# Kernel tuning notes

Hardware: AMD Instinct MI355X
Metric: run time of the kernel (lower is better)

## Reference

```python
import jax, jax.numpy as jnp
import numpy as np

HEADS = 16
D_MODEL = 2048
HEAD_DIM = D_MODEL // HEADS


def setup_inputs() -> dict:
    key = jax.random.key(0)
    ks = jax.random.split(key, 8)
    s = 1.0 / np.sqrt(D_MODEL)
    return {
        "hidden_states": jax.random.normal(ks[0], (2, 2048, D_MODEL), jnp.float32),
        "Wq": jax.random.normal(ks[1], (D_MODEL, D_MODEL), jnp.float32) * s,
        "bq": jax.random.normal(ks[2], (D_MODEL,), jnp.float32) * s,
        "Wk": jax.random.normal(ks[3], (D_MODEL, D_MODEL), jnp.float32) * s,
        "Wv": jax.random.normal(ks[4], (D_MODEL, D_MODEL), jnp.float32) * s,
        "bv": jax.random.normal(ks[5], (D_MODEL,), jnp.float32) * s,
        "Wo": jax.random.normal(ks[6], (D_MODEL, D_MODEL), jnp.float32) * s,
        "bo": jax.random.normal(ks[7], (D_MODEL,), jnp.float32) * s,
    }


def reference(hidden_states, Wq, bq, Wk, Wv, bv, Wo, bo):
    bsz, q_len, _ = hidden_states.shape
    # torch Linear: y = x @ W^T + b; k_W has no bias
    q = hidden_states @ Wq.T + bq
    k = hidden_states @ Wk.T
    v = hidden_states @ Wv.T + bv
    # [b, h, s, d]
    def split_heads(t):
        return t.reshape(bsz, q_len, HEADS, HEAD_DIM).transpose(0, 2, 1, 3)
    q, k, v = split_heads(q), split_heads(k), split_heads(v)
    scale = 1.0 / np.sqrt(HEAD_DIM).astype(np.float32)
    attn_weights = jnp.einsum("bhqd,bhkd->bhqk", q, k) * scale
    attn_weights = jax.nn.softmax(attn_weights, axis=-1)
    attn_output = jnp.einsum("bhqk,bhkd->bhqd", attn_weights, v)
    attn_output = attn_output.transpose(0, 2, 1, 3).reshape(bsz, q_len, D_MODEL)
    attn_output = attn_output @ Wo.T + bo
    return attn_output, attn_weights
```

## Files before the change

kernel.cpp:

```cpp
#include <hip/hip_runtime.h>

typedef _Float16 f16;
typedef _Float16 f16x4 __attribute__((ext_vector_type(4)));
typedef _Float16 f16x8 __attribute__((ext_vector_type(8)));
typedef float f32x4 __attribute__((ext_vector_type(4)));

#define DM 2048
#define NT 4096
#define SEQ 2048
#define HD 128
#define NBH 32
#define QSCALE (0.08838834764831845f * 1.4426950408889634f)

__device__ __forceinline__ void gload16(const f16* g, f16* l) {
  __builtin_amdgcn_global_load_lds(
      (const __attribute__((address_space(1))) void*)g,
      (__attribute__((address_space(3))) void*)l, 16, 0, 0);
}

#define LGKM0                                        \
  asm volatile("s_waitcnt lgkmcnt(0)" ::: "memory"); \
  __builtin_amdgcn_sched_barrier(0)
#define VMC6                                       \
  asm volatile("s_waitcnt vmcnt(6)" ::: "memory"); \
  __builtin_amdgcn_sched_barrier(0)
#define VMC4                                       \
  asm volatile("s_waitcnt vmcnt(4)" ::: "memory"); \
  __builtin_amdgcn_sched_barrier(0)
#define VMC0                                       \
  asm volatile("s_waitcnt vmcnt(0)" ::: "memory"); \
  __builtin_amdgcn_sched_barrier(0)

__global__ __launch_bounds__(256) void cvt_f32_f16(const float* __restrict__ src,
                                                   f16* __restrict__ dst, int n4) {
  int i = blockIdx.x * 256 + threadIdx.x;
  int st = gridDim.x * 256;
  for (; i < n4; i += st) {
    float4 v = ((const float4*)src)[i];
    f16x4 h = {(f16)v.x, (f16)v.y, (f16)v.z, (f16)v.w};
    ((f16x4*)dst)[i] = h;
  }
}

__global__ __launch_bounds__(256) void cvt4_f32_f16(const float* __restrict__ hs,
                                                    const float* __restrict__ s0,
                                                    const float* __restrict__ s1,
                                                    const float* __restrict__ s2,
                                                    f16* __restrict__ hsd,
                                                    f16* __restrict__ wd) {
  int i = blockIdx.x * 256 + threadIdx.x;
  int st = gridDim.x * 256;
  for (; i < 5 * 1048576; i += st) {
    float4 v;
    f16x4 h;
    if (i < 2 * 1048576) {
      v = ((const float4*)hs)[i];
      h[0] = (f16)v.x; h[1] = (f16)v.y; h[2] = (f16)v.z; h[3] = (f16)v.w;
      ((f16x4*)hsd)[i] = h;
    } else {
      const int j = i - 2 * 1048576;
      const int r = j >> 20, jj = j & 1048575;
      const float* s = (r == 0) ? s0 : ((r == 1) ? s1 : s2);
      v = ((const float4*)s)[jj];
      h[0] = (f16)v.x; h[1] = (f16)v.y; h[2] = (f16)v.z; h[3] = (f16)v.w;
      ((f16x4*)wd)[j] = h;
    }
  }
}

template <int MODE>
__global__ __launch_bounds__(512, 2) void gemm8(const f16* __restrict__ A,
                                                const f16* __restrict__ Bm,
                                                const float* __restrict__ bias1,
                                                const float* __restrict__ bias2,
                                                float* __restrict__ outF,
                                                f16* __restrict__ outQ,
                                                f16* __restrict__ outK,
                                                f16* __restrict__ outV) {
  __shared__ __align__(16) f16 smem[73728];
  const int tid = threadIdx.x;
  const int w = tid >> 6, l = tid & 63;
  const int wr = w >> 2, wc = w & 3;
  const int sl = l & 15, t4 = l >> 4;

  const int nbx = gridDim.x;
  const int flat = blockIdx.y * nbx + blockIdx.x;
  const int chunk = (nbx * gridDim.y) >> 3;
  const int swz = (flat & 7) * chunk + (flat >> 3);
  const int row0 = (swz / nbx) * 128, col0 = (swz % nbx) * 256;

  f32x4 acc[4][4] = {};

  const int sr8 = l >> 3;
  const int sch = (l & 7) ^ (sr8 & 7);
  const f16* gA0 = A + (size_t)(row0 + w * 8 + sr8) * DM + sch * 8;
  const f16* gB0 = Bm + (size_t)(col0 + w * 8 + sr8) * DM + sch * 8;

#define SA(tb, kt, r) \
  gload16(gA0 + (size_t)(r) * 64 * DM + (kt) * 64, smem + (tb) * 8192 + (r) * 4096 + w * 512)
#define SB(tb, kt, r)                               \
  gload16(gB0 + (size_t)(r) * 64 * DM + (kt) * 64, \
          smem + 24576 + (tb) * 16384 + (r) * 4096 + w * 512)
#define MF(mi, ni, av, bv) \
  acc[mi][ni] = __builtin_amdgcn_mfma_f32_16x16x32_f16(av, bv, acc[mi][ni], 0, 0, 0)

  const int sx = sl & 7;
  const int sk0 = (t4 ^ sx) * 8;
  const int sk1 = ((4 + t4) ^ sx) * 8;
  const int arow = (wr * 64 + sl) * 64;
  const int brow = (wc * 64 + sl) * 64;

  SA(0, 0, 0); SA(0, 0, 1);
  SB(0, 0, 0); SB(0, 0, 1); SB(0, 0, 2); SB(0, 0, 3);
  SA(1, 1, 0); SA(1, 1, 1);
  SB(1, 1, 0); SB(1, 1, 1); SB(1, 1, 2); SB(1, 1, 3);
  VMC6;
  __builtin_amdgcn_s_barrier();

  int cur = 0;
#pragma unroll 1
  for (int t = 0; t < 32; ++t) {
    const int nb = (cur == 0) ? 2 : cur - 1;
    const bool pf = (t + 2 < 32);
    const int ab = cur * 8192;
    const int bb = 24576 + cur * 16384;
    f16x8 b0, b1, b2, b3, a0, a1;

    b0 = *(const f16x8*)&smem[bb + brow + sk0];
    b1 = *(const f16x8*)&smem[bb + brow + 1024 + sk0];
    b2 = *(const f16x8*)&smem[bb + brow + 2048 + sk0];
    b3 = *(const f16x8*)&smem[bb + brow + 3072 + sk0];
    a0 = *(const f16x8*)&smem[ab + arow + sk0];
    a1 = *(const f16x8*)&smem[ab + arow + 1024 + sk0];
    if (pf) { SA(nb, t + 2, 0); SA(nb, t + 2, 1); }
    __builtin_amdgcn_s_barrier();
    LGKM0;
    __builtin_amdgcn_s_setprio(1);
    MF(0, 0, a0, b0); MF(0, 1, a0, b1); MF(0, 2, a0, b2); MF(0, 3, a0, b3);
    MF(1, 0, a1, b0); MF(1, 1, a1, b1); MF(1, 2, a1, b2); MF(1, 3, a1, b3);
    __builtin_amdgcn_s_setprio(0);
    __builtin_amdgcn_s_barrier();

    a0 = *(const f16x8*)&smem[ab + arow + 2048 + sk0];
    a1 = *(const f16x8*)&smem[ab + arow + 3072 + sk0];
    if (pf) { SB(nb, t + 2, 0); SB(nb, t + 2, 1); }
    __builtin_amdgcn_s_barrier();
    LGKM0;
    __builtin_amdgcn_s_setprio(1);
    MF(2, 0, a0, b0); MF(2, 1, a0, b1); MF(2, 2, a0, b2); MF(2, 3, a0, b3);
    MF(3, 0, a1, b0); MF(3, 1, a1, b1); MF(3, 2, a1, b2); MF(3, 3, a1, b3);
    __builtin_amdgcn_s_setprio(0);
    __builtin_amdgcn_s_barrier();

    b0 = *(const f16x8*)&smem[bb + brow + sk1];
    b1 = *(const f16x8*)&smem[bb + brow + 1024 + sk1];
    b2 = *(const f16x8*)&smem[bb + brow + 2048 + sk1];
    b3 = *(const f16x8*)&smem[bb + brow + 3072 + sk1];
    a0 = *(const f16x8*)&smem[ab + arow + sk1];
    a1 = *(const f16x8*)&smem[ab + arow + 1024 + sk1];
    if (pf) { SB(nb, t + 2, 2); SB(nb, t + 2, 3); }
    __builtin_amdgcn_s_barrier();
    LGKM0;
    __builtin_amdgcn_s_setprio(1);
    MF(0, 0, a0, b0); MF(0, 1, a0, b1); MF(0, 2, a0, b2); MF(0, 3, a0, b3);
    MF(1, 0, a1, b0); MF(1, 1, a1, b1); MF(1, 2, a1, b2); MF(1, 3, a1, b3);
    __builtin_amdgcn_s_setprio(0);
    __builtin_amdgcn_s_barrier();

    a0 = *(const f16x8*)&smem[ab + arow + 2048 + sk1];
    a1 = *(const f16x8*)&smem[ab + arow + 3072 + sk1];
    __builtin_amdgcn_s_barrier();
    LGKM0;
    __builtin_amdgcn_s_setprio(1);
    MF(2, 0, a0, b0); MF(2, 1, a0, b1); MF(2, 2, a0, b2); MF(2, 3, a0, b3);
    MF(3, 0, a1, b0); MF(3, 1, a1, b1); MF(3, 2, a1, b2); MF(3, 3, a1, b3);
    __builtin_amdgcn_s_setprio(0);
    if (t < 30) { VMC6; } else { VMC0; }
    __builtin_amdgcn_s_barrier();
    cur = (cur == 2) ? 0 : cur + 1;
  }
#undef SA
#undef SB
#undef MF

  const int rl0 = wr * 64 + t4 * 4;
  const int cl0 = wc * 64 + sl;
  if constexpr (MODE == 0) {
#pragma unroll
    for (int mi = 0; mi < 4; mi++) {
#pragma unroll
      for (int ni = 0; ni < 4; ni++) {
        const int col = col0 + cl0 + ni * 16;
        const float bi = bias1[col];
#pragma unroll
        for (int j = 0; j < 4; j++) {
          const int row = row0 + rl0 + mi * 16 + j;
          outF[(size_t)row * DM + col] = acc[mi][ni][j] + bi;
        }
      }
    }
  } else {
    const int region = col0 >> 11;
    const int c2 = col0 & 2047;
    __syncthreads();
    if (region == 2) {
#pragma unroll
      for (int mi = 0; mi < 4; mi++)
#pragma unroll
        for (int ni = 0; ni < 4; ni++) {
          const int cl = cl0 + ni * 16;
          const float bb2 = bias2[c2 + cl];
#pragma unroll
          for (int j = 0; j < 4; j++)
            smem[cl * 136 + rl0 + mi * 16 + j] = (f16)(acc[mi][ni][j] + bb2);
        }
      __syncthreads();
      const int b = row0 >> 11, s0 = row0 & 2047;
#pragma unroll
      for (int it = 0; it < 8; ++it) {
        const int ck = it * 512 + tid;
        const int ci = ck >> 4, cc = (ck & 15) * 8;
        const int dg = c2 + ci;
        *(f16x8*)&outV[((size_t)(b * 16 + (dg >> 7)) * HD + (dg & 127)) * SEQ + s0 + cc] =
            *(const f16x8*)&smem[ci * 136 + cc];
      }
    } else {
#pragma unroll
      for (int mi = 0; mi < 4; mi++)
#pragma unroll
        for (int ni = 0; ni < 4; ni++) {
          const int cl = cl0 + ni * 16;
          const int cg = c2 + cl;
          const float badd = (region == 0) ? bias1[cg] : 0.0f;
#pragma unroll
          for (int j = 0; j < 4; j++) {
            float v = acc[mi][ni][j] + badd;
            if (region == 0) v *= QSCALE;
            smem[(rl0 + mi * 16 + j) * 264 + cl] = (f16)v;
          }
        }
      __syncthreads();
      f16* const dst = (region == 0 ? outQ : outK) + (size_t)row0 * DM + c2;
#pragma unroll
      for (int it = 0; it < 8; ++it) {
        const int ck = it * 512 + tid;
        const int rr = ck >> 5, cc = (ck & 31) * 8;
        *(f16x8*)&dst[(size_t)rr * DM + cc] = *(const f16x8*)&smem[rr * 264 + cc];
      }
    }
  }
}

__global__ __launch_bounds__(256, 2) void attn(const f16* __restrict__ Q,
                                               const f16* __restrict__ Kt,
                                               const f16* __restrict__ Vt,
                                               float* __restrict__ Pout,
                                               f16* __restrict__ Oout) {
  __shared__ __align__(16) f16 smem[36864];
  f16* const lP = smem + 32768;

  const int tid = threadIdx.x, w = tid >> 6, l = tid & 63;
  const int t = l >> 4, sl = l & 15, t8 = l >> 3, sl8 = l & 7;

  const int flat = blockIdx.y * gridDim.x + blockIdx.x;
  const int swz = (flat & 7) * 128 + (flat >> 3);
  const int bh = swz >> 5, q0 = (swz & 31) * 64;

  const int b = bh >> 4, h = bh & 15;
  const f16* Qg = Q + (size_t)(b * SEQ) * DM + h * HD;
  const f16* Kg = Kt + (size_t)(b * SEQ) * DM + h * HD;
  const f16* Vg = Vt + (size_t)bh * HD * SEQ;

#pragma unroll
  for (int c = 0; c < 4; c++) {
    const int row = w * 16 + c * 4 + t;
    const int ch = sl ^ (row & 7);
    gload16(Qg + (size_t)(q0 + row) * DM + ch * 8, smem + 16384 + w * 2048 + c * 512);
    gload16(Kg + (size_t)row * DM + ch * 8, smem + w * 2048 + c * 512);
    gload16(Kg + (size_t)(64 + row) * DM + ch * 8, smem + 8192 + w * 2048 + c * 512);
  }
  __syncthreads();

  f16x8 qf[4];
  {
    const int row = w * 16 + sl;
#pragma unroll
    for (int g = 0; g < 4; g++) {
      const int ch = (g * 4 + t) ^ (row & 7);
      qf[g] = *(const f16x8*)&smem[16384 + row * 128 + ch * 8];
    }
  }
  LGKM0;
  __builtin_amdgcn_s_barrier();

  float lsum = 0.0f;

  for (int kb = 0; kb < 32; ++kb) {
    f16* const kc = smem + (kb & 3) * 8192;
    if (kb + 2 < 32) {
      f16* const kn = smem + ((kb + 2) & 3) * 8192;
#pragma unroll
      for (int c = 0; c < 4; c++) {
        const int row = w * 16 + c * 4 + t;
        const int ch = sl ^ (row & 7);
        gload16(Kg + (size_t)((kb + 2) * 64 + row) * DM + ch * 8, kn + w * 2048 + c * 512);
      }
    }
#pragma unroll
    for (int cb = 0; cb < 4; ++cb) {
      f32x4 s = {0.f, 0.f, 0.f, 0.f};
      const int key = cb * 16 + sl;
#pragma unroll
      for (int g = 0; g < 4; ++g) {
        const int ch = (g * 4 + t) ^ (key & 7);
        f16x8 kf = *(const f16x8*)&kc[key * 128 + ch * 8];
        s = __builtin_amdgcn_mfma_f32_16x16x32_f16(kf, qf[g], s, 0, 0, 0);
      }
#pragma unroll
      for (int j = 0; j < 4; j++) lsum += __builtin_amdgcn_exp2f(s[j]);
    }
    if (kb < 31) {
      if (kb + 2 < 32) { VMC4; } else { VMC0; }
      __builtin_amdgcn_s_barrier();
    }
  }
  lsum += __shfl_xor(lsum, 16);
  lsum += __shfl_xor(lsum, 32);
  const float inv = 1.0f / lsum;

  {
#pragma unroll
    for (int c = 0; c < 4; c++) {
      const int row = w * 16 + c * 4 + t;
      const int ch = sl ^ (row & 7);
      gload16(Kg + (size_t)row * DM + ch * 8, smem + w * 2048 + c * 512);
    }
#pragma unroll
    for (int c = 0; c < 4; c++) {
      const int row = w * 32 + c * 8 + t8;
      const int ch = sl8 ^ (row & 7);
      gload16(Vg + (size_t)row * SEQ + ch * 8, smem + 16384 + w * 2048 + c * 512);
    }
  }
  __syncthreads();

  f32x4 oacc[8] = {};
  const int qrow = w * 16 + sl;
  float* const Prow = Pout + ((size_t)bh * SEQ + q0 + qrow) * SEQ;

  for (int kb = 0; kb < 32; ++kb) {
    f16* const kc = smem + (kb & 1) * 8192;
    f16* const vc = smem + 16384 + (kb & 1) * 8192;
    if (kb < 31) {
      f16* const kn = smem + ((kb + 1) & 1) * 8192;
      f16* const vn = smem + 16384 + ((kb + 1) & 1) * 8192;
#pragma unroll
      for (int c = 0; c < 4; c++) {
        const int row = w * 16 + c * 4 + t;
        const int ch = sl ^ (row & 7);
        gload16(Kg + (size_t)((kb + 1) * 64 + row) * DM + ch * 8, kn + w * 2048 + c * 512);
      }
#pragma unroll
      for (int c = 0; c < 4; c++) {
        const int row = w * 32 + c * 8 + t8;
        const int ch = sl8 ^ (row & 7);
        gload16(Vg + (size_t)row * SEQ + (kb + 1) * 64 + ch * 8, vn + w * 2048 + c * 512);
      }
    }
#pragma unroll
    for (int cb = 0; cb < 4; ++cb) {
      f32x4 s = {0.f, 0.f, 0.f, 0.f};
      const int key = cb * 16 + sl;
#pragma unroll
      for (int g = 0; g < 4; ++g) {
        const int ch = (g * 4 + t) ^ (key & 7);
        f16x8 kf = *(const f16x8*)&kc[key * 128 + ch * 8];
        s = __builtin_amdgcn_mfma_f32_16x16x32_f16(kf, qf[g], s, 0, 0, 0);
      }
      f32x4 p4;
      f16x4 ph;
#pragma unroll
      for (int j = 0; j < 4; j++) {
        const float p = __builtin_amdgcn_exp2f(s[j]) * inv;
        p4[j] = p;
        ph[j] = (f16)p;
      }
      __builtin_nontemporal_store(p4, (f32x4*)(Prow + kb * 64 + cb * 16 + t * 4));
      const int chs = (cb * 2 + (t >> 1)) ^ (qrow & 7);
      *(f16x4*)&lP[qrow * 64 + chs * 8 + (t & 1) * 4] = ph;
    }
    f16x8 pf[2];
#pragma unroll
    for (int ks = 0; ks < 2; ++ks) {
      const int ch = (ks * 4 + t) ^ (qrow & 7);
      pf[ks] = *(const f16x8*)&lP[qrow * 64 + ch * 8];
    }
    __builtin_amdgcn_s_setprio(1);
#pragma unroll
    for (int cb = 0; cb < 8; ++cb) {
      const int d = cb * 16 + sl;
#pragma unroll
      for (int ks = 0; ks < 2; ++ks) {
        const int ch = (ks * 4 + t) ^ (d & 7);
        f16x8 vf = *(const f16x8*)&vc[d * 64 + ch * 8];
        oacc[cb] = __builtin_amdgcn_mfma_f32_16x16x32_f16(pf[ks], vf, oacc[cb], 0, 0, 0);
      }
    }
    __builtin_amdgcn_s_setprio(0);
    if (kb < 31) {
      VMC4;
      __builtin_amdgcn_s_barrier();
    }
  }

#pragma unroll
  for (int cb = 0; cb < 8; ++cb) {
    const int d = cb * 16 + sl;
#pragma unroll
    for (int j = 0; j < 4; j++) {
      const int lrow = w * 16 + t * 4 + j;
      Oout[((size_t)(b * SEQ + q0 + lrow)) * DM + h * HD + d] = (f16)oacc[cb][j];
    }
  }
}

extern "C" void kernel_launch(void* const* d_in, const int* in_sizes, int n_in,
                              void* d_out, int out_size, void* d_ws, size_t ws_size,
                              hipStream_t stream) {
  const float* hs = (const float*)d_in[0];
  const float* Wq = (const float*)d_in[1];
  const float* bq = (const float*)d_in[2];
  const float* Wk = (const float*)d_in[3];
  const float* Wv = (const float*)d_in[4];
  const float* bv = (const float*)d_in[5];
  const float* Wo = (const float*)d_in[6];
  const float* bo = (const float*)d_in[7];
  float* out = (float*)d_out;
  float* Pout = out + (size_t)NT * DM;

  f16* q16 = (f16*)d_ws;
  f16* k16 = q16 + (size_t)NT * DM;
  f16* vt16 = k16 + (size_t)NT * DM;
  f16* ao16 = vt16 + (size_t)NT * DM;
  f16* hs16 = (f16*)Pout;
  f16* wqkv16 = hs16 + (size_t)NT * DM;
  f16* wo16 = q16;

  cvt4_f32_f16<<<2048, 256, 0, stream>>>(hs, Wq, Wk, Wv, hs16, wqkv16);

  gemm8<3><<<dim3(6144 / 256, NT / 128), 512, 0, stream>>>(
      hs16, wqkv16, bq, bv, nullptr, q16, k16, vt16);

  attn<<<dim3(SEQ / 64, NBH), 256, 0, stream>>>(q16, k16, vt16, Pout, ao16);

  cvt_f32_f16<<<1024, 256, 0, stream>>>(Wo, wo16, DM * DM / 4);
  gemm8<0><<<dim3(DM / 256, NT / 128), 512, 0, stream>>>(
      ao16, wo16, bo, nullptr, out, nullptr, nullptr, nullptr);
}
```

Before: 379.9 us.

## Process 128 query rows per attention block to reuse K/V tiles

The attention kernel now gives each block 128 query rows instead of 64, so each wave handles two 16-row query tiles. Every K and V fragment read from LDS feeds MFMAs for both tiles, which halves global K/V traffic and LDS reads per query row. The launch grid is halved, LDS grows to hold the larger Q staging and P buffers, and the K ring-buffer slots are remapped so the first K tiles don't overlap the Q staging area. In exchange the kernel needs more registers for a second set of Q fragments and accumulators, and has fewer blocks to fill the GPU.

```diff
diff --git a/kernel.cpp b/kernel.cpp
--- a/kernel.cpp
+++ b/kernel.cpp
@@ -20,6 +20,9 @@
 
 #define LGKM0                                        \
   asm volatile("s_waitcnt lgkmcnt(0)" ::: "memory"); \
+  __builtin_amdgcn_sched_barrier(0)
+#define VMC8                                       \
+  asm volatile("s_waitcnt vmcnt(8)" ::: "memory"); \
   __builtin_amdgcn_sched_barrier(0)
 #define VMC6                                       \
   asm volatile("s_waitcnt vmcnt(6)" ::: "memory"); \
@@ -256,15 +259,15 @@
                                                const f16* __restrict__ Vt,
                                                float* __restrict__ Pout,
                                                f16* __restrict__ Oout) {
-  __shared__ __align__(16) f16 smem[36864];
+  __shared__ __align__(16) f16 smem[40960];
   f16* const lP = smem + 32768;
 
   const int tid = threadIdx.x, w = tid >> 6, l = tid & 63;
   const int t = l >> 4, sl = l & 15, t8 = l >> 3, sl8 = l & 7;
 
   const int flat = blockIdx.y * gridDim.x + blockIdx.x;
-  const int swz = (flat & 7) * 128 + (flat >> 3);
-  const int bh = swz >> 5, q0 = (swz & 31) * 64;
+  const int swz = (flat & 7) * 64 + (flat >> 3);
+  const int bh = swz >> 4, q0 = (swz & 15) * 128;
 
   const int b = bh >> 4, h = bh & 15;
   const f16* Qg = Q + (size_t)(b * SEQ) * DM + h * HD;
@@ -272,33 +275,40 @@
   const f16* Vg = Vt + (size_t)bh * HD * SEQ;
 
 #pragma unroll
+  for (int c = 0; c < 8; c++) {
+    const int row = w * 32 + c * 4 + t;
+    const int ch = sl ^ (row & 7);
+    gload16(Qg + (size_t)(q0 + row) * DM + ch * 8, smem + w * 4096 + c * 512);
+  }
+#pragma unroll
   for (int c = 0; c < 4; c++) {
     const int row = w * 16 + c * 4 + t;
     const int ch = sl ^ (row & 7);
-    gload16(Qg + (size_t)(q0 + row) * DM + ch * 8, smem + 16384 + w * 2048 + c * 512);
-    gload16(Kg + (size_t)row * DM + ch * 8, smem + w * 2048 + c * 512);
-    gload16(Kg + (size_t)(64 + row) * DM + ch * 8, smem + 8192 + w * 2048 + c * 512);
+    gload16(Kg + (size_t)row * DM + ch * 8, smem + 16384 + w * 2048 + c * 512);
+    gload16(Kg + (size_t)(64 + row) * DM + ch * 8, smem + 24576 + w * 2048 + c * 512);
   }
   __syncthreads();
 
-  f16x8 qf[4];
-  {
-    const int row = w * 16 + sl;
+  f16x8 qf[2][4];
+#pragma unroll
+  for (int u = 0; u < 2; u++) {
+    const int row = w * 32 + u * 16 + sl;
 #pragma unroll
     for (int g = 0; g < 4; g++) {
       const int ch = (g * 4 + t) ^ (row & 7);
-      qf[g] = *(const f16x8*)&smem[16384 + row * 128 + ch * 8];
+      qf[u][g] = *(const f16x8*)&smem[row * 128 + ch * 8];
     }
   }
   LGKM0;
   __builtin_amdgcn_s_barrier();
 
-  float lsum = 0.0f;
-
+  float lsum[2] = {0.0f, 0.0f};
+
+#pragma unroll 1
   for (int kb = 0; kb < 32; ++kb) {
-    f16* const kc = smem + (kb & 3) * 8192;
+    f16* const kc = smem + ((kb + 2) & 3) * 8192;
     if (kb + 2 < 32) {
-      f16* const kn = smem + ((kb + 2) & 3) * 8192;
+      f16* const kn = smem + (kb & 3) * 8192;
 #pragma unroll
       for (int c = 0; c < 4; c++) {
         const int row = w * 16 + c * 4 + t;
@@ -308,46 +318,52 @@
     }
 #pragma unroll
     for (int cb = 0; cb < 4; ++cb) {
-      f32x4 s = {0.f, 0.f, 0.f, 0.f};
       const int key = cb * 16 + sl;
-#pragma unroll
-      for (int g = 0; g < 4; ++g) {
-        const int ch = (g * 4 + t) ^ (key & 7);
-        f16x8 kf = *(const f16x8*)&kc[key * 128 + ch * 8];
-        s = __builtin_amdgcn_mfma_f32_16x16x32_f16(kf, qf[g], s, 0, 0, 0);
-      }
-#pragma unroll
-      for (int j = 0; j < 4; j++) lsum += __builtin_amdgcn_exp2f(s[j]);
+      f16x8 kf[4];
+#pragma unroll
+      for (int g = 0; g < 4; ++g)
+        kf[g] = *(const f16x8*)&kc[key * 128 + (((g * 4 + t) ^ (key & 7)) * 8)];
+#pragma unroll
+      for (int u = 0; u < 2; ++u) {
+        f32x4 s = {0.f, 0.f, 0.f, 0.f};
+#pragma unroll
+        for (int g = 0; g < 4; ++g)
+          s = __builtin_amdgcn_mfma_f32_16x16x32_f16(kf[g], qf[u][g], s, 0, 0, 0);
+#pragma unroll
+        for (int j = 0; j < 4; j++) lsum[u] += __builtin_amdgcn_exp2f(s[j]);
+      }
     }
     if (kb < 31) {
       if (kb + 2 < 32) { VMC4; } else { VMC0; }
       __builtin_amdgcn_s_barrier();
     }
   }
-  lsum += __shfl_xor(lsum, 16);
-  lsum += __shfl_xor(lsum, 32);
-  const float inv = 1.0f / lsum;
-
-  {
-#pragma unroll
-    for (int c = 0; c < 4; c++) {
-      const int row = w * 16 + c * 4 + t;
-      const int ch = sl ^ (row & 7);
-      gload16(Kg + (size_t)row * DM + ch * 8, smem + w * 2048 + c * 512);
-    }
-#pragma unroll
-    for (int c = 0; c < 4; c++) {
-      const int row = w * 32 + c * 8 + t8;
-      const int ch = sl8 ^ (row & 7);
-      gload16(Vg + (size_t)row * SEQ + ch * 8, smem + 16384 + w * 2048 + c * 512);
-    }
+  float inv[2];
+#pragma unroll
+  for (int u = 0; u < 2; u++) {
+    float v = lsum[u];
+    v += __shfl_xor(v, 16);
+    v += __shfl_xor(v, 32);
+    inv[u] = 1.0f / v;
+  }
+
+#pragma unroll
+  for (int c = 0; c < 4; c++) {
+    const int row = w * 16 + c * 4 + t;
+    const int ch = sl ^ (row & 7);
+    gload16(Kg + (size_t)row * DM + ch * 8, smem + w * 2048 + c * 512);
+  }
+#pragma unroll
+  for (int c = 0; c < 4; c++) {
+    const int row = w * 32 + c * 8 + t8;
+    const int ch = sl8 ^ (row & 7);
+    gload16(Vg + (size_t)row * SEQ + ch * 8, smem + 16384 + w * 2048 + c * 512);
   }
   __syncthreads();
 
-  f32x4 oacc[8] = {};
-  const int qrow = w * 16 + sl;
-  float* const Prow = Pout + ((size_t)bh * SEQ + q0 + qrow) * SEQ;
-
+  f32x4 oacc[2][8] = {};
+
+#pragma unroll 1
   for (int kb = 0; kb < 32; ++kb) {
     f16* const kc = smem + (kb & 1) * 8192;
     f16* const vc = smem + 16384 + (kb & 1) * 8192;
@@ -369,57 +385,71 @@
     }
 #pragma unroll
     for (int cb = 0; cb < 4; ++cb) {
-      f32x4 s = {0.f, 0.f, 0.f, 0.f};
       const int key = cb * 16 + sl;
-#pragma unroll
-      for (int g = 0; g < 4; ++g) {
-        const int ch = (g * 4 + t) ^ (key & 7);
-        f16x8 kf = *(const f16x8*)&kc[key * 128 + ch * 8];
-        s = __builtin_amdgcn_mfma_f32_16x16x32_f16(kf, qf[g], s, 0, 0, 0);
-      }
-      f32x4 p4;
-      f16x4 ph;
-#pragma unroll
-      for (int j = 0; j < 4; j++) {
-        const float p = __builtin_amdgcn_exp2f(s[j]) * inv;
-        p4[j] = p;
-        ph[j] = (f16)p;
-      }
-      __builtin_nontemporal_store(p4, (f32x4*)(Prow + kb * 64 + cb * 16 + t * 4));
-      const int chs = (cb * 2 + (t >> 1)) ^ (qrow & 7);
-      *(f16x4*)&lP[qrow * 64 + chs * 8 + (t & 1) * 4] = ph;
-    }
-    f16x8 pf[2];
-#pragma unroll
-    for (int ks = 0; ks < 2; ++ks) {
-      const int ch = (ks * 4 + t) ^ (qrow & 7);
-      pf[ks] = *(const f16x8*)&lP[qrow * 64 + ch * 8];
+      f16x8 kf[4];
+#pragma unroll
+      for (int g = 0; g < 4; ++g)
+        kf[g] = *(const f16x8*)&kc[key * 128 + (((g * 4 + t) ^ (key & 7)) * 8)];
+#pragma unroll
+      for (int u = 0; u < 2; ++u) {
+        f32x4 s = {0.f, 0.f, 0.f, 0.f};
+#pragma unroll
+        for (int g = 0; g < 4; ++g)
+          s = __builtin_amdgcn_mfma_f32_16x16x32_f16(kf[g], qf[u][g], s, 0, 0, 0);
+        f32x4 p4;
+        f16x4 ph;
+#pragma unroll
+        for (int j = 0; j < 4; j++) {
+          const float p = __builtin_amdgcn_exp2f(s[j]) * inv[u];
+          p4[j] = p;
+          ph[j] = (f16)p;
+        }
+        const int qrow = w * 32 + u * 16 + sl;
+        __builtin_nontemporal_store(
+            p4, (f32x4*)(Pout + ((size_t)bh * SEQ + q0 + qrow) * SEQ + kb * 64 + cb * 16 + t * 4));
+        const int chs = (cb * 2 + (t >> 1)) ^ (qrow & 7);
+        *(f16x4*)&lP[qrow * 64 + chs * 8 + (t & 1) * 4] = ph;
+      }
+    }
+    f16x8 pf[2][2];
+#pragma unroll
+    for (int u = 0; u < 2; ++u) {
+      const int qrow = w * 32 + u * 16 + sl;
+#pragma unroll
+      for (int ks = 0; ks < 2; ++ks) {
+        const int ch = (ks * 4 + t) ^ (qrow & 7);
+        pf[u][ks] = *(const f16x8*)&lP[qrow * 64 + ch * 8];
+      }
     }
     __builtin_amdgcn_s_setprio(1);
 #pragma unroll
-    for (int cb = 0; cb < 8; ++cb) {
-      const int d = cb * 16 + sl;
-#pragma unroll
-      for (int ks = 0; ks < 2; ++ks) {
-        const int ch = (ks * 4 + t) ^ (d & 7);
-        f16x8 vf = *(const f16x8*)&vc[d * 64 + ch * 8];
-        oacc[cb] = __builtin_amdgcn_mfma_f32_16x16x32_f16(pf[ks], vf, oacc[cb], 0, 0, 0);
+    for (int db = 0; db < 8; ++db) {
+      const int d = db * 16 + sl;
+      f16x8 vf0 = *(const f16x8*)&vc[d * 64 + ((t ^ (d & 7)) * 8)];
+      f16x8 vf1 = *(const f16x8*)&vc[d * 64 + (((4 + t) ^ (d & 7)) * 8)];
+#pragma unroll
+      for (int u = 0; u < 2; ++u) {
+        oacc[u][db] = __builtin_amdgcn_mfma_f32_16x16x32_f16(pf[u][0], vf0, oacc[u][db], 0, 0, 0);
+        oacc[u][db] = __builtin_amdgcn_mfma_f32_16x16x32_f16(pf[u][1], vf1, oacc[u][db], 0, 0, 0);
       }
     }
     __builtin_amdgcn_s_setprio(0);
     if (kb < 31) {
-      VMC4;
+      VMC8;
       __builtin_amdgcn_s_barrier();
     }
   }
 
 #pragma unroll
-  for (int cb = 0; cb < 8; ++cb) {
-    const int d = cb * 16 + sl;
-#pragma unroll
-    for (int j = 0; j < 4; j++) {
-      const int lrow = w * 16 + t * 4 + j;
-      Oout[((size_t)(b * SEQ + q0 + lrow)) * DM + h * HD + d] = (f16)oacc[cb][j];
+  for (int u = 0; u < 2; ++u) {
+#pragma unroll
+    for (int db = 0; db < 8; ++db) {
+      const int d = db * 16 + sl;
+#pragma unroll
+      for (int j = 0; j < 4; j++) {
+        const int lrow = w * 32 + u * 16 + t * 4 + j;
+        Oout[((size_t)(b * SEQ + q0 + lrow)) * DM + h * HD + d] = (f16)oacc[u][db][j];
+      }
     }
   }
 }
@@ -451,7 +481,7 @@
   gemm8<3><<<dim3(6144 / 256, NT / 128), 512, 0, stream>>>(
       hs16, wqkv16, bq, bv, nullptr, q16, k16, vt16);
 
-  attn<<<dim3(SEQ / 64, NBH), 256, 0, stream>>>(q16, k16, vt16, Pout, ao16);
+  attn<<<dim3(SEQ / 128, NBH), 256, 0, stream>>>(q16, k16, vt16, Pout, ao16);
 
   cvt_f32_f16<<<1024, 256, 0, stream>>>(Wo, wo16, DM * DM / 4);
   gemm8<0><<<dim3(DM / 256, NT / 128), 512, 0, stream>>>(
```

After: 393.7 us. 3.6% more time.
